# Performance work log

Measured on AMD Instinct MI355X. Metric: run time of the kernel, lower is better.

Reference implementation:

```python
import jax, jax.numpy as jnp
import numpy as np

B, T, D, H = 4, 2048, 1024, 2048   # batch, seq, d_model, moe_dim
E, S, K = 8, 2, 2                   # routed experts, shared experts, top_k


def setup_inputs() -> dict:
    key = jax.random.key(0)
    ks = jax.random.split(key, 10)
    s = 0.02  # init scale
    return {
        "x": jax.random.normal(ks[0], (B, T, D), jnp.float32),
        "gate_w": jax.random.normal(ks[1], (D, E), jnp.float32) * s,
        "gate_b": jnp.zeros((E,), jnp.float32),
        # routed experts, stacked over expert axis
        "rw1": jax.random.normal(ks[2], (E, D, H), jnp.float32) * s,
        "rb1": jnp.zeros((E, H), jnp.float32),
        "rw2": jax.random.normal(ks[3], (E, D, H), jnp.float32) * s,
        "rb2": jnp.zeros((E, H), jnp.float32),
        "rw3": jax.random.normal(ks[4], (E, H, D), jnp.float32) * s,
        "rb3": jnp.zeros((E, D), jnp.float32),
        # shared experts, stacked
        "sw1": jax.random.normal(ks[5], (S, D, H), jnp.float32) * s,
        "sb1": jnp.zeros((S, H), jnp.float32),
        "sw2": jax.random.normal(ks[6], (S, D, H), jnp.float32) * s,
        "sb2": jnp.zeros((S, H), jnp.float32),
        "sw3": jax.random.normal(ks[7], (S, H, D), jnp.float32) * s,
        "sb3": jnp.zeros((S, D), jnp.float32),
    }


def _swiglu_stacked(x, w1, b1, w2, b2, w3, b3):
    # x: (B,T,D); w1/w2: (N,D,H); w3: (N,H,D) -> out: (N,B,T,D)
    p1 = jnp.einsum('btd,ndh->nbth', x, w1) + b1[:, None, None, :]
    p2 = jnp.einsum('btd,ndh->nbth', x, w2) + b2[:, None, None, :]
    glu = jax.nn.silu(p1) * p2
    return jnp.einsum('nbth,nhd->nbtd', glu, w3) + b3[:, None, None, :]


def reference(x, gate_w, gate_b, rw1, rb1, rw2, rb2, rw3, rb3,
              sw1, sb1, sw2, sb2, sw3, sb3):
    # Gate: softmax over all routed experts, then top-k (no renormalization)
    scores = jax.nn.softmax(x @ gate_w + gate_b, axis=-1)      # (B,T,E)
    weights, indices = jax.lax.top_k(scores, K)                # (B,T,K)

    # Routed experts: compute all experts densely (same math as the naive
    # masked-dense torch loop), then gather top-k outputs per token.
    routed_all = _swiglu_stacked(x, rw1, rb1, rw2, rb2, rw3, rb3)  # (E,B,T,D)
    out_bted = jnp.transpose(routed_all, (1, 2, 0, 3))             # (B,T,E,D)
    gathered = jnp.take_along_axis(out_bted, indices[..., None], axis=2)  # (B,T,K,D)
    routed = jnp.sum(weights[..., None] * gathered, axis=2)        # (B,T,D)

    # Shared experts: mean over shared experts
    shared = _swiglu_stacked(x, sw1, sb1, sw2, sb2, sw3, sb3).mean(axis=0)

    return shared + routed
```

## Files before the change

### kernel.cpp

```cpp
#include <hip/hip_runtime.h>
#include <math.h>

#define TOKENS   8192
#define DMODEL   1024
#define HDIM     2048
#define NEXP     8
#define NSH      2
#define NGRP     10
#define R_ROUTED 16384
#define R_TOTAL  32768

typedef float  f32x4  __attribute__((ext_vector_type(4)));
typedef __bf16 bf16x8 __attribute__((ext_vector_type(8)));
typedef unsigned short u16x8 __attribute__((ext_vector_type(8)));

typedef __attribute__((address_space(1))) const void as1_void;
typedef __attribute__((address_space(3))) void as3_void;
#define GLOAD16(g, l) __builtin_amdgcn_global_load_lds((as1_void*)(g), (as3_void*)(l), 16, 0, 0)

__device__ __forceinline__ unsigned short f2bf(float f) {
  unsigned int u = __float_as_uint(f);
  u += 0x7fffu + ((u >> 16) & 1u);
  return (unsigned short)(u >> 16);
}
__device__ __forceinline__ float bf2f(unsigned short u) {
  return __uint_as_float(((unsigned int)u) << 16);
}


__global__ __launch_bounds__(256) void convert_x_kernel(const float* __restrict__ x,
                                                        unsigned short* __restrict__ xb) {
  int i = blockIdx.x * blockDim.x + threadIdx.x;
  const float4 v = reinterpret_cast<const float4*>(x)[i];
  ushort4 o;
  o.x = f2bf(v.x); o.y = f2bf(v.y); o.z = f2bf(v.z); o.w = f2bf(v.w);
  reinterpret_cast<ushort4*>(xb)[i] = o;
}

__global__ __launch_bounds__(256) void transpose_cvt64_kernel(const float* __restrict__ src,
                                                              unsigned short* __restrict__ dst,
                                                              int R, int C) {
  __shared__ float tile[64][65];
  const size_t mat = blockIdx.z;
  src += mat * (size_t)R * C;
  dst += mat * (size_t)R * C;
  const int c0 = blockIdx.x * 64, r0 = blockIdx.y * 64;
  const int tid = threadIdx.x;
  const int tx = tid & 15, ty = tid >> 4;
  #pragma unroll
  for (int rr = 0; rr < 4; ++rr) {
    const int row = ty + rr * 16;
    const float4 v = *reinterpret_cast<const float4*>(&src[(size_t)(r0 + row) * C + c0 + tx * 4]);
    tile[row][tx * 4 + 0] = v.x;
    tile[row][tx * 4 + 1] = v.y;
    tile[row][tx * 4 + 2] = v.z;
    tile[row][tx * 4 + 3] = v.w;
  }
  __syncthreads();
  const int oc = tid >> 2, og = tid & 3;
  u16x8 u0, u1;
  #pragma unroll
  for (int e = 0; e < 8; ++e) u0[e] = f2bf(tile[og * 16 + e][oc]);
  #pragma unroll
  for (int e = 0; e < 8; ++e) u1[e] = f2bf(tile[og * 16 + 8 + e][oc]);
  unsigned short* dp = &dst[(size_t)(c0 + oc) * R + r0 + og * 16];
  *reinterpret_cast<u16x8*>(dp) = u0;
  *reinterpret_cast<u16x8*>(dp + 8) = u1;
}


__global__ __launch_bounds__(64) void gate_kernel(const float* __restrict__ x,
                                                  const float* __restrict__ gw,
                                                  const float* __restrict__ gb,
                                                  int* __restrict__ topk_idx,
                                                  float* __restrict__ topk_w,
                                                  int* __restrict__ counts) {
  const int t = blockIdx.x;
  const int lane = threadIdx.x;
  const float* xr = x + (size_t)t * DMODEL;
  float acc[NEXP];
  #pragma unroll
  for (int e = 0; e < NEXP; ++e) acc[e] = 0.f;
  for (int d = lane; d < DMODEL; d += 64) {
    const float xv = xr[d];
    const float* g = gw + (size_t)d * NEXP;
    #pragma unroll
    for (int e = 0; e < NEXP; ++e) acc[e] += xv * g[e];
  }
  #pragma unroll
  for (int e = 0; e < NEXP; ++e) {
    float v = acc[e];
    v += __shfl_down(v, 32); v += __shfl_down(v, 16); v += __shfl_down(v, 8);
    v += __shfl_down(v, 4);  v += __shfl_down(v, 2);  v += __shfl_down(v, 1);
    acc[e] = v;
  }
  if (lane == 0) {
    float p[NEXP];
    float mx = -1e30f;
    #pragma unroll
    for (int e = 0; e < NEXP; ++e) { acc[e] += gb[e]; mx = fmaxf(mx, acc[e]); }
    float s = 0.f;
    #pragma unroll
    for (int e = 0; e < NEXP; ++e) { p[e] = expf(acc[e] - mx); s += p[e]; }
    const float inv = 1.f / s;
    #pragma unroll
    for (int e = 0; e < NEXP; ++e) p[e] *= inv;
    int i1 = 0; float v1 = p[0];
    #pragma unroll
    for (int e = 1; e < NEXP; ++e) if (p[e] > v1) { v1 = p[e]; i1 = e; }
    int i2 = -1; float v2 = -1e30f;
    #pragma unroll
    for (int e = 0; e < NEXP; ++e) if (e != i1 && p[e] > v2) { v2 = p[e]; i2 = e; }
    topk_idx[t * 2 + 0] = i1; topk_w[t * 2 + 0] = v1;
    topk_idx[t * 2 + 1] = i2; topk_w[t * 2 + 1] = v2;
    atomicAdd(&counts[i1], 1);
    atomicAdd(&counts[i2], 1);
  }
}

__global__ void offs_kernel(const int* __restrict__ counts, int* __restrict__ offs) {
  if (threadIdx.x == 0 && blockIdx.x == 0) {
    int cum = 0;
    for (int e = 0; e < NEXP; ++e) { offs[e] = cum; cum += counts[e]; }
    offs[8] = R_ROUTED;
    offs[9] = R_ROUTED + TOKENS;
    offs[10] = R_TOTAL;
  }
}

__global__ __launch_bounds__(256) void scatter_kernel(const int* __restrict__ topk_idx,
                                                      const int* __restrict__ offs,
                                                      int* __restrict__ cursors,
                                                      int* __restrict__ row_token,
                                                      int* __restrict__ tok_rows) {
  const int t = blockIdx.x * blockDim.x + threadIdx.x;
  if (t >= TOKENS) return;
  #pragma unroll
  for (int k = 0; k < 2; ++k) {
    const int e = topk_idx[t * 2 + k];
    const int pos = atomicAdd(&cursors[e], 1);
    const int r = offs[e] + pos;
    row_token[r] = t;
    tok_rows[t * 2 + k] = r;
  }
  row_token[R_ROUTED + t] = t;
  row_token[R_ROUTED + TOKENS + t] = t;
}


__global__ __launch_bounds__(256, 3) void gemm1_kernel(
    const unsigned short* __restrict__ xb,
    const unsigned short* __restrict__ w1t,
    const unsigned short* __restrict__ w2t,
    const float* __restrict__ rb1, const float* __restrict__ sb1,
    const float* __restrict__ rb2, const float* __restrict__ sb2,
    const int* __restrict__ offs,
    const int* __restrict__ row_token,
    unsigned short* __restrict__ glu) {
  const int g = blockIdx.z;
  const int off_g = offs[g];
  const int n_g = offs[g + 1] - off_g;
  const int m0 = blockIdx.x * 128;
  if (m0 >= n_g) return;
  const int n0 = blockIdx.y * 64;

  __shared__ __align__(16) unsigned short Abuf[128 * 64];
  __shared__ __align__(16) unsigned short B1buf[64 * 64];
  __shared__ __align__(16) unsigned short B2buf[64 * 64];

  const int tid = threadIdx.x;
  const int lane = tid & 63;
  const int wid = tid >> 6;
  const int wm = wid >> 1, wn = wid & 1;
  const int l15 = lane & 15, kq = lane >> 4;

  const unsigned short* w1g = w1t + (size_t)g * HDIM * DMODEL;
  const unsigned short* w2g = w2t + (size_t)g * HDIM * DMODEL;

  const unsigned short* srcA[4]; int dA[4];
  #pragma unroll
  for (int r = 0; r < 4; ++r) {
    const int chunk = r * 256 + tid, row = chunk >> 3, j = chunk & 7;
    int ar = m0 + row; if (ar > n_g - 1) ar = n_g - 1;
    srcA[r] = xb + (size_t)row_token[off_g + ar] * DMODEL + ((j ^ (row & 7)) << 3);
    dA[r] = (r * 256 + (tid & ~63)) << 3;
  }
  const unsigned short* srcB1[2]; const unsigned short* srcB2[2]; int dB[2];
  #pragma unroll
  for (int r = 0; r < 2; ++r) {
    const int chunk = r * 256 + tid, row = chunk >> 3, j = chunk & 7;
    const size_t o = (size_t)(n0 + row) * DMODEL + ((j ^ (row & 7)) << 3);
    srcB1[r] = w1g + o; srcB2[r] = w2g + o;
    dB[r] = (r * 256 + (tid & ~63)) << 3;
  }

  f32x4 acc1[4][2], acc2[4][2];
  const f32x4 zero = {0.f, 0.f, 0.f, 0.f};
  #pragma unroll
  for (int i = 0; i < 4; ++i)
    #pragma unroll
    for (int j = 0; j < 2; ++j) { acc1[i][j] = zero; acc2[i][j] = zero; }

  for (int k0 = 0; k0 < DMODEL; k0 += 64) {
    __syncthreads();
    #pragma unroll
    for (int r = 0; r < 4; ++r) GLOAD16(srcA[r] + k0, &Abuf[dA[r]]);
    #pragma unroll
    for (int r = 0; r < 2; ++r) {
      GLOAD16(srcB1[r] + k0, &B1buf[dB[r]]);
      GLOAD16(srcB2[r] + k0, &B2buf[dB[r]]);
    }
    __syncthreads();
    #pragma unroll
    for (int ks = 0; ks < 2; ++ks) {
      const int kc = ks * 4 + kq;
      bf16x8 a[4], p[2], q[2];
      #pragma unroll
      for (int mi = 0; mi < 4; ++mi) {
        const int row = wm * 64 + mi * 16 + l15;
        a[mi] = *reinterpret_cast<const bf16x8*>(&Abuf[row * 64 + ((kc ^ (row & 7)) << 3)]);
      }
      #pragma unroll
      for (int ni = 0; ni < 2; ++ni) {
        const int row = wn * 32 + ni * 16 + l15;
        const int ko = (kc ^ (row & 7)) << 3;
        p[ni] = *reinterpret_cast<const bf16x8*>(&B1buf[row * 64 + ko]);
        q[ni] = *reinterpret_cast<const bf16x8*>(&B2buf[row * 64 + ko]);
      }
      #pragma unroll
      for (int mi = 0; mi < 4; ++mi)
        #pragma unroll
        for (int ni = 0; ni < 2; ++ni) {
          acc1[mi][ni] = __builtin_amdgcn_mfma_f32_16x16x32_bf16(a[mi], p[ni], acc1[mi][ni], 0, 0, 0);
          acc2[mi][ni] = __builtin_amdgcn_mfma_f32_16x16x32_bf16(a[mi], q[ni], acc2[mi][ni], 0, 0, 0);
        }
    }
  }

  const float* b1p = (g < NEXP) ? (rb1 + (size_t)g * HDIM) : (sb1 + (size_t)(g - NEXP) * HDIM);
  const float* b2p = (g < NEXP) ? (rb2 + (size_t)g * HDIM) : (sb2 + (size_t)(g - NEXP) * HDIM);

  #pragma unroll
  for (int mi = 0; mi < 4; ++mi) {
    #pragma unroll
    for (int r = 0; r < 4; ++r) {
      const int m = m0 + wm * 64 + mi * 16 + kq * 4 + r;
      if (m < n_g) {
        #pragma unroll
        for (int ni = 0; ni < 2; ++ni) {
          const int n = n0 + wn * 32 + ni * 16 + l15;
          const float x1 = acc1[mi][ni][r] + b1p[n];
          const float x2 = acc2[mi][ni][r] + b2p[n];
          glu[(size_t)(off_g + m) * HDIM + n] = f2bf((x1 / (1.f + expf(-x1))) * x2);
        }
      }
    }
  }
}


__global__ __launch_bounds__(256, 3) void gemm2_kernel(
    const unsigned short* __restrict__ glu,
    const unsigned short* __restrict__ w3t,
    const float* __restrict__ rb3, const float* __restrict__ sb3,
    const int* __restrict__ offs,
    unsigned short* __restrict__ y) {
  const int g = blockIdx.z;
  const int off_g = offs[g];
  const int n_g = offs[g + 1] - off_g;
  const int m0 = blockIdx.x * 128;
  if (m0 >= n_g) return;
  const int n0 = blockIdx.y * 128;

  __shared__ __align__(16) unsigned short Abuf[128 * 64];
  __shared__ __align__(16) unsigned short Bbuf[128 * 64];

  const int tid = threadIdx.x;
  const int lane = tid & 63;
  const int wid = tid >> 6;
  const int wm = wid >> 1, wn = wid & 1;
  const int l15 = lane & 15, kq = lane >> 4;

  const unsigned short* w3g = w3t + (size_t)g * DMODEL * HDIM;

  const unsigned short* srcA[4]; const unsigned short* srcB[4]; int dAB[4];
  #pragma unroll
  for (int r = 0; r < 4; ++r) {
    const int chunk = r * 256 + tid, row = chunk >> 3, j = chunk & 7;
    int ar = m0 + row; if (ar > n_g - 1) ar = n_g - 1;
    srcA[r] = glu + (size_t)(off_g + ar) * HDIM + ((j ^ (row & 7)) << 3);
    srcB[r] = w3g + (size_t)(n0 + row) * HDIM + ((j ^ (row & 7)) << 3);
    dAB[r] = (r * 256 + (tid & ~63)) << 3;
  }

  f32x4 acc[4][4];
  const f32x4 zero = {0.f, 0.f, 0.f, 0.f};
  #pragma unroll
  for (int i = 0; i < 4; ++i)
    #pragma unroll
    for (int j = 0; j < 4; ++j) acc[i][j] = zero;

  for (int k0 = 0; k0 < HDIM; k0 += 64) {
    __syncthreads();
    #pragma unroll
    for (int r = 0; r < 4; ++r) {
      GLOAD16(srcA[r] + k0, &Abuf[dAB[r]]);
      GLOAD16(srcB[r] + k0, &Bbuf[dAB[r]]);
    }
    __syncthreads();
    #pragma unroll
    for (int ks = 0; ks < 2; ++ks) {
      const int kc = ks * 4 + kq;
      bf16x8 a[4], b[4];
      #pragma unroll
      for (int mi = 0; mi < 4; ++mi) {
        const int row = wm * 64 + mi * 16 + l15;
        a[mi] = *reinterpret_cast<const bf16x8*>(&Abuf[row * 64 + ((kc ^ (row & 7)) << 3)]);
      }
      #pragma unroll
      for (int ni = 0; ni < 4; ++ni) {
        const int row = wn * 64 + ni * 16 + l15;
        b[ni] = *reinterpret_cast<const bf16x8*>(&Bbuf[row * 64 + ((kc ^ (row & 7)) << 3)]);
      }
      #pragma unroll
      for (int mi = 0; mi < 4; ++mi)
        #pragma unroll
        for (int ni = 0; ni < 4; ++ni)
          acc[mi][ni] = __builtin_amdgcn_mfma_f32_16x16x32_bf16(a[mi], b[ni], acc[mi][ni], 0, 0, 0);
    }
  }

  const float* b3p = (g < NEXP) ? (rb3 + (size_t)g * DMODEL) : (sb3 + (size_t)(g - NEXP) * DMODEL);

  #pragma unroll
  for (int mi = 0; mi < 4; ++mi) {
    #pragma unroll
    for (int r = 0; r < 4; ++r) {
      const int m = m0 + wm * 64 + mi * 16 + kq * 4 + r;
      if (m < n_g) {
        unsigned short* yrow = y + (size_t)(off_g + m) * DMODEL;
        #pragma unroll
        for (int ni = 0; ni < 4; ++ni) {
          const int n = n0 + wn * 64 + ni * 16 + l15;
          yrow[n] = f2bf(acc[mi][ni][r] + b3p[n]);
        }
      }
    }
  }
}


__global__ __launch_bounds__(256) void reduce_kernel(const unsigned short* __restrict__ y,
                                                     const int* __restrict__ tok_rows,
                                                     const float* __restrict__ topk_w,
                                                     float* __restrict__ out) {
  const int t = blockIdx.x * 2 + (threadIdx.x >> 7);
  const int col = (threadIdx.x & 127) * 8;
  const int r0 = tok_rows[t * 2 + 0], r1 = tok_rows[t * 2 + 1];
  const float w0 = topk_w[t * 2 + 0], w1 = topk_w[t * 2 + 1];

  float o[8];
  #pragma unroll
  for (int e = 0; e < 8; ++e) o[e] = 0.f;
  auto addrow = [&](const unsigned short* p, float w) {
    const u16x8 v = *reinterpret_cast<const u16x8*>(p);
    #pragma unroll
    for (int e = 0; e < 8; ++e) o[e] += w * bf2f(v[e]);
  };
  addrow(y + (size_t)r0 * DMODEL + col, w0);
  addrow(y + (size_t)r1 * DMODEL + col, w1);
  addrow(y + (size_t)(R_ROUTED + t) * DMODEL + col, 0.5f);
  addrow(y + (size_t)(R_ROUTED + TOKENS + t) * DMODEL + col, 0.5f);

  float4* op = reinterpret_cast<float4*>(out + (size_t)t * DMODEL + col);
  op[0] = make_float4(o[0], o[1], o[2], o[3]);
  op[1] = make_float4(o[4], o[5], o[6], o[7]);
}


extern "C" void kernel_launch(void* const* d_in, const int* in_sizes, int n_in,
                              void* d_out, int out_size, void* d_ws, size_t ws_size,
                              hipStream_t stream) {
  const float* x      = (const float*)d_in[0];
  const float* gate_w = (const float*)d_in[1];
  const float* gate_b = (const float*)d_in[2];
  const float* rw1    = (const float*)d_in[3];
  const float* rb1    = (const float*)d_in[4];
  const float* rw2    = (const float*)d_in[5];
  const float* rb2    = (const float*)d_in[6];
  const float* rw3    = (const float*)d_in[7];
  const float* rb3    = (const float*)d_in[8];
  const float* sw1    = (const float*)d_in[9];
  const float* sb1    = (const float*)d_in[10];
  const float* sw2    = (const float*)d_in[11];
  const float* sb2    = (const float*)d_in[12];
  const float* sw3    = (const float*)d_in[13];
  const float* sb3    = (const float*)d_in[14];
  float* out = (float*)d_out;

  const size_t XB_OFF   = 0;
  const size_t W1T_OFF  = XB_OFF  + (size_t)TOKENS * DMODEL * 2;
  const size_t W2T_OFF  = W1T_OFF + (size_t)NGRP * HDIM * DMODEL * 2;
  const size_t W3T_OFF  = W2T_OFF + (size_t)NGRP * HDIM * DMODEL * 2;
  const size_t GLU_OFF  = W3T_OFF + (size_t)NGRP * DMODEL * HDIM * 2;
  const size_t Y_OFF    = W1T_OFF;
  const size_t RTOK_OFF = GLU_OFF + (size_t)R_TOTAL * HDIM * 2;
  const size_t TKI_OFF  = RTOK_OFF + (size_t)R_TOTAL * 4;
  const size_t TKW_OFF  = TKI_OFF + (size_t)TOKENS * 2 * 4;
  const size_t TRW_OFF  = TKW_OFF + (size_t)TOKENS * 2 * 4;
  const size_t META_OFF = TRW_OFF + (size_t)TOKENS * 2 * 4;
  const size_t NEED     = META_OFF + 256;
  if (ws_size < NEED) return;

  char* ws = (char*)d_ws;
  unsigned short* xb   = (unsigned short*)(ws + XB_OFF);
  unsigned short* w1t  = (unsigned short*)(ws + W1T_OFF);
  unsigned short* w2t  = (unsigned short*)(ws + W2T_OFF);
  unsigned short* w3t  = (unsigned short*)(ws + W3T_OFF);
  unsigned short* glu  = (unsigned short*)(ws + GLU_OFF);
  unsigned short* yy   = (unsigned short*)(ws + Y_OFF);
  int*   row_token = (int*)(ws + RTOK_OFF);
  int*   topk_idx  = (int*)(ws + TKI_OFF);
  float* topk_w    = (float*)(ws + TKW_OFF);
  int*   tok_rows  = (int*)(ws + TRW_OFF);
  int*   counts    = (int*)(ws + META_OFF);
  int*   offs      = counts + 16;
  int*   cursors   = counts + 32;

  hipMemsetAsync(counts, 0, 192, stream);

  convert_x_kernel<<<TOKENS * DMODEL / 4 / 256, 256, 0, stream>>>(x, xb);

  transpose_cvt64_kernel<<<dim3(HDIM / 64, DMODEL / 64, NEXP), 256, 0, stream>>>(rw1, w1t, DMODEL, HDIM);
  transpose_cvt64_kernel<<<dim3(HDIM / 64, DMODEL / 64, NSH), 256, 0, stream>>>(
      sw1, w1t + (size_t)NEXP * HDIM * DMODEL, DMODEL, HDIM);
  transpose_cvt64_kernel<<<dim3(HDIM / 64, DMODEL / 64, NEXP), 256, 0, stream>>>(rw2, w2t, DMODEL, HDIM);
  transpose_cvt64_kernel<<<dim3(HDIM / 64, DMODEL / 64, NSH), 256, 0, stream>>>(
      sw2, w2t + (size_t)NEXP * HDIM * DMODEL, DMODEL, HDIM);
  transpose_cvt64_kernel<<<dim3(DMODEL / 64, HDIM / 64, NEXP), 256, 0, stream>>>(rw3, w3t, HDIM, DMODEL);
  transpose_cvt64_kernel<<<dim3(DMODEL / 64, HDIM / 64, NSH), 256, 0, stream>>>(
      sw3, w3t + (size_t)NEXP * DMODEL * HDIM, HDIM, DMODEL);

  gate_kernel<<<TOKENS, 64, 0, stream>>>(x, gate_w, gate_b, topk_idx, topk_w, counts);
  offs_kernel<<<1, 64, 0, stream>>>(counts, offs);
  scatter_kernel<<<TOKENS / 256, 256, 0, stream>>>(topk_idx, offs, cursors,
                                                   row_token, tok_rows);

  gemm1_kernel<<<dim3(TOKENS / 128, HDIM / 64, NGRP), 256, 0, stream>>>(
      xb, w1t, w2t, rb1, sb1, rb2, sb2, offs, row_token, glu);
  gemm2_kernel<<<dim3(TOKENS / 128, DMODEL / 128, NGRP), 256, 0, stream>>>(
      glu, w3t, rb3, sb3, offs, yy);
  reduce_kernel<<<TOKENS / 2, 256, 0, stream>>>(yy, tok_rows, topk_w, out);
}
```

Before: 1.040 ms.

## Triple-buffer LDS loads and enlarge M tiles in grouped MoE GEMMs

Both grouped GEMM kernels move to 512-thread blocks covering 256 rows. Their main loop becomes a 3-stage software pipeline: async global-to-LDS loads for tile k+2 are issued before computing tile k, with explicit vmcnt waits and a single barrier per iteration. The aim is to hide global load latency behind MFMA work and cut the per-tile double __syncthreads cost. In exchange, each block now needs about 147KB of LDS, which likely limits a CU to one block and lowers occupancy. Larger M tiles also waste more work on partially filled expert groups.

Result: slower. 1.937 ms (+86.3%).

```diff
diff --git a/kernel.cpp b/kernel.cpp
--- a/kernel.cpp
+++ b/kernel.cpp
@@ -17,6 +17,10 @@
 typedef __attribute__((address_space(1))) const void as1_void;
 typedef __attribute__((address_space(3))) void as3_void;
 #define GLOAD16(g, l) __builtin_amdgcn_global_load_lds((as1_void*)(g), (as3_void*)(l), 16, 0, 0)
+
+#define WAITV6() asm volatile("s_waitcnt vmcnt(6)" ::: "memory")
+#define WAITV0() asm volatile("s_waitcnt vmcnt(0)" ::: "memory")
+#define SBAR()   do { __builtin_amdgcn_s_barrier(); asm volatile("" ::: "memory"); } while (0)
 
 __device__ __forceinline__ unsigned short f2bf(float f) {
   unsigned int u = __float_as_uint(f);
@@ -148,7 +152,7 @@
 }
 
 
-__global__ __launch_bounds__(256, 3) void gemm1_kernel(
+__global__ __launch_bounds__(512, 2) void gemm1_kernel(
     const unsigned short* __restrict__ xb,
     const unsigned short* __restrict__ w1t,
     const unsigned short* __restrict__ w2t,
@@ -160,13 +164,13 @@
   const int g = blockIdx.z;
   const int off_g = offs[g];
   const int n_g = offs[g + 1] - off_g;
-  const int m0 = blockIdx.x * 128;
+  const int m0 = blockIdx.x * 256;
   if (m0 >= n_g) return;
   const int n0 = blockIdx.y * 64;
 
-  __shared__ __align__(16) unsigned short Abuf[128 * 64];
-  __shared__ __align__(16) unsigned short B1buf[64 * 64];
-  __shared__ __align__(16) unsigned short B2buf[64 * 64];
+  __shared__ __align__(16) unsigned short Abuf[3][256 * 64];
+  __shared__ __align__(16) unsigned short B1buf[3][64 * 64];
+  __shared__ __align__(16) unsigned short B2buf[3][64 * 64];
 
   const int tid = threadIdx.x;
   const int lane = tid & 63;
@@ -180,18 +184,17 @@
   const unsigned short* srcA[4]; int dA[4];
   #pragma unroll
   for (int r = 0; r < 4; ++r) {
-    const int chunk = r * 256 + tid, row = chunk >> 3, j = chunk & 7;
+    const int chunk = r * 512 + tid, row = chunk >> 3, j = chunk & 7;
     int ar = m0 + row; if (ar > n_g - 1) ar = n_g - 1;
     srcA[r] = xb + (size_t)row_token[off_g + ar] * DMODEL + ((j ^ (row & 7)) << 3);
-    dA[r] = (r * 256 + (tid & ~63)) << 3;
-  }
-  const unsigned short* srcB1[2]; const unsigned short* srcB2[2]; int dB[2];
-  #pragma unroll
-  for (int r = 0; r < 2; ++r) {
-    const int chunk = r * 256 + tid, row = chunk >> 3, j = chunk & 7;
+    dA[r] = (r * 512 + (tid & ~63)) << 3;
+  }
+  const unsigned short* srcB1; const unsigned short* srcB2; int dB;
+  {
+    const int row = tid >> 3, j = tid & 7;
     const size_t o = (size_t)(n0 + row) * DMODEL + ((j ^ (row & 7)) << 3);
-    srcB1[r] = w1g + o; srcB2[r] = w2g + o;
-    dB[r] = (r * 256 + (tid & ~63)) << 3;
+    srcB1 = w1g + o; srcB2 = w2g + o;
+    dB = (tid & ~63) << 3;
   }
 
   f32x4 acc1[4][2], acc2[4][2];
@@ -201,16 +204,13 @@
     #pragma unroll
     for (int j = 0; j < 2; ++j) { acc1[i][j] = zero; acc2[i][j] = zero; }
 
-  for (int k0 = 0; k0 < DMODEL; k0 += 64) {
-    __syncthreads();
-    #pragma unroll
-    for (int r = 0; r < 4; ++r) GLOAD16(srcA[r] + k0, &Abuf[dA[r]]);
-    #pragma unroll
-    for (int r = 0; r < 2; ++r) {
-      GLOAD16(srcB1[r] + k0, &B1buf[dB[r]]);
-      GLOAD16(srcB2[r] + k0, &B2buf[dB[r]]);
-    }
-    __syncthreads();
+  auto stage = [&](int b, int k0) {
+    #pragma unroll
+    for (int r = 0; r < 4; ++r) GLOAD16(srcA[r] + k0, &Abuf[b][dA[r]]);
+    GLOAD16(srcB1 + k0, &B1buf[b][dB]);
+    GLOAD16(srcB2 + k0, &B2buf[b][dB]);
+  };
+  auto compute = [&](int b) {
     #pragma unroll
     for (int ks = 0; ks < 2; ++ks) {
       const int kc = ks * 4 + kq;
@@ -218,14 +218,14 @@
       #pragma unroll
       for (int mi = 0; mi < 4; ++mi) {
         const int row = wm * 64 + mi * 16 + l15;
-        a[mi] = *reinterpret_cast<const bf16x8*>(&Abuf[row * 64 + ((kc ^ (row & 7)) << 3)]);
+        a[mi] = *reinterpret_cast<const bf16x8*>(&Abuf[b][row * 64 + ((kc ^ (row & 7)) << 3)]);
       }
       #pragma unroll
       for (int ni = 0; ni < 2; ++ni) {
         const int row = wn * 32 + ni * 16 + l15;
         const int ko = (kc ^ (row & 7)) << 3;
-        p[ni] = *reinterpret_cast<const bf16x8*>(&B1buf[row * 64 + ko]);
-        q[ni] = *reinterpret_cast<const bf16x8*>(&B2buf[row * 64 + ko]);
+        p[ni] = *reinterpret_cast<const bf16x8*>(&B1buf[b][row * 64 + ko]);
+        q[ni] = *reinterpret_cast<const bf16x8*>(&B2buf[b][row * 64 + ko]);
       }
       #pragma unroll
       for (int mi = 0; mi < 4; ++mi)
@@ -235,6 +235,21 @@
           acc2[mi][ni] = __builtin_amdgcn_mfma_f32_16x16x32_bf16(a[mi], q[ni], acc2[mi][ni], 0, 0, 0);
         }
     }
+  };
+
+  stage(0, 0);
+  stage(1, 64);
+  WAITV6();
+  SBAR();
+
+  #define NT1 (DMODEL / 64)
+  for (int kt = 0; kt < NT1; ++kt) {
+    const int cur = kt % 3;
+    if (kt + 2 < NT1) stage((kt + 2) % 3, (kt + 2) * 64);
+    compute(cur);
+    if (kt + 2 < NT1)      { WAITV6(); }
+    else if (kt + 1 < NT1) { WAITV0(); }
+    if (kt + 1 < NT1) SBAR();
   }
 
   const float* b1p = (g < NEXP) ? (rb1 + (size_t)g * HDIM) : (sb1 + (size_t)(g - NEXP) * HDIM);
@@ -259,7 +274,7 @@
 }
 
 
-__global__ __launch_bounds__(256, 3) void gemm2_kernel(
+__global__ __launch_bounds__(512, 2) void gemm2_kernel(
     const unsigned short* __restrict__ glu,
     const unsigned short* __restrict__ w3t,
     const float* __restrict__ rb3, const float* __restrict__ sb3,
@@ -268,12 +283,12 @@
   const int g = blockIdx.z;
   const int off_g = offs[g];
   const int n_g = offs[g + 1] - off_g;
-  const int m0 = blockIdx.x * 128;
+  const int m0 = blockIdx.x * 256;
   if (m0 >= n_g) return;
   const int n0 = blockIdx.y * 128;
 
-  __shared__ __align__(16) unsigned short Abuf[128 * 64];
-  __shared__ __align__(16) unsigned short Bbuf[128 * 64];
+  __shared__ __align__(16) unsigned short Abuf[3][256 * 64];
+  __shared__ __align__(16) unsigned short Bbuf[3][128 * 64];
 
   const int tid = threadIdx.x;
   const int lane = tid & 63;
@@ -283,14 +298,20 @@
 
   const unsigned short* w3g = w3t + (size_t)g * DMODEL * HDIM;
 
-  const unsigned short* srcA[4]; const unsigned short* srcB[4]; int dAB[4];
+  const unsigned short* srcA[4]; int dA[4];
   #pragma unroll
   for (int r = 0; r < 4; ++r) {
-    const int chunk = r * 256 + tid, row = chunk >> 3, j = chunk & 7;
+    const int chunk = r * 512 + tid, row = chunk >> 3, j = chunk & 7;
     int ar = m0 + row; if (ar > n_g - 1) ar = n_g - 1;
     srcA[r] = glu + (size_t)(off_g + ar) * HDIM + ((j ^ (row & 7)) << 3);
+    dA[r] = (r * 512 + (tid & ~63)) << 3;
+  }
+  const unsigned short* srcB[2]; int dB[2];
+  #pragma unroll
+  for (int r = 0; r < 2; ++r) {
+    const int chunk = r * 512 + tid, row = chunk >> 3, j = chunk & 7;
     srcB[r] = w3g + (size_t)(n0 + row) * HDIM + ((j ^ (row & 7)) << 3);
-    dAB[r] = (r * 256 + (tid & ~63)) << 3;
+    dB[r] = (r * 512 + (tid & ~63)) << 3;
   }
 
   f32x4 acc[4][4];
@@ -300,34 +321,48 @@
     #pragma unroll
     for (int j = 0; j < 4; ++j) acc[i][j] = zero;
 
-  for (int k0 = 0; k0 < HDIM; k0 += 64) {
-    __syncthreads();
-    #pragma unroll
-    for (int r = 0; r < 4; ++r) {
-      GLOAD16(srcA[r] + k0, &Abuf[dAB[r]]);
-      GLOAD16(srcB[r] + k0, &Bbuf[dAB[r]]);
-    }
-    __syncthreads();
+  auto stage = [&](int b, int k0) {
+    #pragma unroll
+    for (int r = 0; r < 4; ++r) GLOAD16(srcA[r] + k0, &Abuf[b][dA[r]]);
+    #pragma unroll
+    for (int r = 0; r < 2; ++r) GLOAD16(srcB[r] + k0, &Bbuf[b][dB[r]]);
+  };
+  auto compute = [&](int b) {
     #pragma unroll
     for (int ks = 0; ks < 2; ++ks) {
       const int kc = ks * 4 + kq;
-      bf16x8 a[4], b[4];
+      bf16x8 a[4], bb[4];
       #pragma unroll
       for (int mi = 0; mi < 4; ++mi) {
         const int row = wm * 64 + mi * 16 + l15;
-        a[mi] = *reinterpret_cast<const bf16x8*>(&Abuf[row * 64 + ((kc ^ (row & 7)) << 3)]);
+        a[mi] = *reinterpret_cast<const bf16x8*>(&Abuf[b][row * 64 + ((kc ^ (row & 7)) << 3)]);
       }
       #pragma unroll
       for (int ni = 0; ni < 4; ++ni) {
         const int row = wn * 64 + ni * 16 + l15;
-        b[ni] = *reinterpret_cast<const bf16x8*>(&Bbuf[row * 64 + ((kc ^ (row & 7)) << 3)]);
+        bb[ni] = *reinterpret_cast<const bf16x8*>(&Bbuf[b][row * 64 + ((kc ^ (row & 7)) << 3)]);
       }
       #pragma unroll
       for (int mi = 0; mi < 4; ++mi)
         #pragma unroll
         for (int ni = 0; ni < 4; ++ni)
-          acc[mi][ni] = __builtin_amdgcn_mfma_f32_16x16x32_bf16(a[mi], b[ni], acc[mi][ni], 0, 0, 0);
+          acc[mi][ni] = __builtin_amdgcn_mfma_f32_16x16x32_bf16(a[mi], bb[ni], acc[mi][ni], 0, 0, 0);
     }
+  };
+
+  stage(0, 0);
+  stage(1, 64);
+  WAITV6();
+  SBAR();
+
+  #define NT2 (HDIM / 64)
+  for (int kt = 0; kt < NT2; ++kt) {
+    const int cur = kt % 3;
+    if (kt + 2 < NT2) stage((kt + 2) % 3, (kt + 2) * 64);
+    compute(cur);
+    if (kt + 2 < NT2)      { WAITV6(); }
+    else if (kt + 1 < NT2) { WAITV0(); }
+    if (kt + 1 < NT2) SBAR();
   }
 
   const float* b3p = (g < NEXP) ? (rb3 + (size_t)g * DMODEL) : (sb3 + (size_t)(g - NEXP) * DMODEL);
@@ -446,9 +481,9 @@
   scatter_kernel<<<TOKENS / 256, 256, 0, stream>>>(topk_idx, offs, cursors,
                                                    row_token, tok_rows);
 
-  gemm1_kernel<<<dim3(TOKENS / 128, HDIM / 64, NGRP), 256, 0, stream>>>(
+  gemm1_kernel<<<dim3(TOKENS / 256, HDIM / 64, NGRP), 512, 0, stream>>>(
       xb, w1t, w2t, rb1, sb1, rb2, sb2, offs, row_token, glu);
-  gemm2_kernel<<<dim3(TOKENS / 128, DMODEL / 128, NGRP), 256, 0, stream>>>(
+  gemm2_kernel<<<dim3(TOKENS / 256, DMODEL / 128, NGRP), 512, 0, stream>>>(
       glu, w3t, rb3, sb3, offs, yy);
   reduce_kernel<<<TOKENS / 2, 256, 0, stream>>>(yy, tok_rows, topk_w, out);
 }
```
